# Optimization experiments

Hardware: AMD Instinct MI355X
Metric: run time of the kernel (lower is better)

## Reference

```python
import jax, jax.numpy as jnp
import numpy as np

WINDOW_SIZE = 11
SIGMA = 1.5
C1 = 0.01 ** 2
C2 = 0.03 ** 2


def _gaussian_window(size, sigma):
    coords = jnp.arange(size, dtype=jnp.float32) - (size - 1) / 2
    g = jnp.exp(-(coords ** 2) / (2 * sigma ** 2))
    g = g / g.sum()
    return g[:, None] * g[None, :]  # [size, size]


def _depthwise_conv(x, w2d):
    # x: [B, C, H, W]; w2d: [k, k] shared Gaussian window
    C = x.shape[1]
    k = w2d.shape[0]
    rhs = jnp.broadcast_to(w2d[None, None], (C, 1, k, k)).astype(x.dtype)
    pad = k // 2
    return jax.lax.conv_general_dilated(
        x, rhs,
        window_strides=(1, 1),
        padding=[(pad, pad), (pad, pad)],
        dimension_numbers=('NCHW', 'OIHW', 'NCHW'),
        feature_group_count=C,
    )


def setup_inputs() -> dict:
    key = jax.random.key(0)
    k1, k2 = jax.random.split(key)
    pred = jax.random.uniform(k1, (16, 3, 512, 512), dtype=jnp.float32)
    target = jax.random.uniform(k2, (16, 3, 512, 512), dtype=jnp.float32)
    return {"pred": pred, "target": target}


def reference(pred, target):
    w = _gaussian_window(WINDOW_SIZE, SIGMA)
    mu_x = _depthwise_conv(pred, w)
    mu_y = _depthwise_conv(target, w)
    s_x = _depthwise_conv(pred ** 2, w) - mu_x ** 2
    s_y = _depthwise_conv(target ** 2, w) - mu_y ** 2
    s_xy = _depthwise_conv(pred * target, w) - mu_x * mu_y
    ssim = ((2 * mu_x * mu_y + C1) * (2 * s_xy + C2)
            / ((mu_x ** 2 + mu_y ** 2 + C1) * (s_x + s_y + C2)))
    return 1.0 - ssim.mean()
```

## Files before the change

### kernel.cpp

```cpp
#include <hip/hip_runtime.h>
#include <math.h>

#define IMG_H 512
#define IMG_W 512
#define NPLANE 48
#define NXT 8
#define NSEG 8
#define NTASK (NPLANE*NXT*NSEG)
#define NPIX 12582912.0

__global__ void ssim_zero_kernel(double* acc) {
    if (threadIdx.x == 0) acc[0] = 0.0;
}

__global__ __launch_bounds__(256)
void ssim_main_kernel(const float* __restrict__ pred,
                      const float* __restrict__ targ,
                      double* __restrict__ acc,
                      float w0, float w1, float w2,
                      float w3, float w4, float w5) {
    const int wid  = (blockIdx.x << 2) + (threadIdx.x >> 6);
    const int lane = threadIdx.x & 63;
    const int xt   = wid & 7;
    const int yseg = (wid >> 3) & 7;
    const int pl   = wid >> 6;
    const int x    = (xt << 6) + lane;
    const int y0   = yseg << 6;

    const float* __restrict__ pb = pred + (size_t)pl * (IMG_H * IMG_W);
    const float* __restrict__ tb = targ + (size_t)pl * (IMG_H * IMG_W);

#define WSYM(M) ((M)==0||(M)==10 ? w0 : (M)==1||(M)==9 ? w1 :               \
                 (M)==2||(M)==8  ? w2 : (M)==3||(M)==7 ? w3 :               \
                 (M)==4||(M)==6  ? w4 : w5)

#define DECL_TAP(K)                                                          \
    const int   cq##K = x + (K) - 5;                                         \
    const int   cx##K = cq##K < 0 ? 0 : (cq##K > IMG_W - 1 ? IMG_W - 1 : cq##K); \
    const float wv##K = ((unsigned)cq##K < (unsigned)IMG_W) ? WSYM(K) : 0.f;
    DECL_TAP(0) DECL_TAP(1) DECL_TAP(2) DECL_TAP(3) DECL_TAP(4) DECL_TAP(5)
    DECL_TAP(6) DECL_TAP(7) DECL_TAP(8) DECL_TAP(9) DECL_TAP(10)
#undef DECL_TAP

#define DECL_RING(F) float F##0, F##1, F##2, F##3, F##4, F##5, F##6, F##7, F##8, F##9, F##10;
    DECL_RING(rmx) DECL_RING(rmy) DECL_RING(rxx) DECL_RING(ryy) DECL_RING(rxy)
#undef DECL_RING

#define HTAP(K) {                                                            \
    const float p  = pr[cx##K];                                              \
    const float t  = tr[cx##K];                                              \
    const float wp = wv##K * p;                                              \
    const float wt = wv##K * t;                                              \
    amx += wp; amy += wt;                                                    \
    axx = fmaf(wp, p, axx);                                                  \
    ayy = fmaf(wt, t, ayy);                                                  \
    axy = fmaf(wp, t, axy); }

#define HROW(YV, S) do {                                                     \
    const int y_ = (YV);                                                     \
    float amx = 0.f, amy = 0.f, axx = 0.f, ayy = 0.f, axy = 0.f;             \
    if ((unsigned)y_ < (unsigned)IMG_H) {           \
        const float* __restrict__ pr = pb + y_ * IMG_W;                      \
        const float* __restrict__ tr = tb + y_ * IMG_W;                      \
        HTAP(0) HTAP(1) HTAP(2) HTAP(3) HTAP(4) HTAP(5)                      \
        HTAP(6) HTAP(7) HTAP(8) HTAP(9) HTAP(10)                             \
    }                                                                        \
    rmx##S = amx; rmy##S = amy;                                              \
    rxx##S = axx; ryy##S = ayy; rxy##S = axy;                                \
} while (0)

    HROW(y0 - 5, 0); __builtin_amdgcn_sched_barrier(0);
    HROW(y0 - 4, 1); __builtin_amdgcn_sched_barrier(0);
    HROW(y0 - 3, 2); __builtin_amdgcn_sched_barrier(0);
    HROW(y0 - 2, 3); __builtin_amdgcn_sched_barrier(0);
    HROW(y0 - 1, 4); __builtin_amdgcn_sched_barrier(0);
    HROW(y0 + 0, 5); __builtin_amdgcn_sched_barrier(0);
    HROW(y0 + 1, 6); __builtin_amdgcn_sched_barrier(0);
    HROW(y0 + 2, 7); __builtin_amdgcn_sched_barrier(0);
    HROW(y0 + 3, 8); __builtin_amdgcn_sched_barrier(0);
    HROW(y0 + 4, 9); __builtin_amdgcn_sched_barrier(0);

    const float C1 = 0.0001f;
    const float C2 = 0.0009f;
    float sum = 0.f;

#define VTAP(JJ, S) {                                                        \
    const float wk = WSYM(((S) + 11 - (JJ)) % 11);                           \
    mx = fmaf(wk, rmx##S, mx);                                               \
    my = fmaf(wk, rmy##S, my);                                               \
    xx = fmaf(wk, rxx##S, xx);                                               \
    yy = fmaf(wk, ryy##S, yy);                                               \
    xy = fmaf(wk, rxy##S, xy); }

#define PHASE(JJ, SNEW) do {                                                 \
    const int j_ = c * 11 + (JJ);                                            \
    HROW(y0 + 5 + j_, SNEW);                                                 \
    float mx = 0.f, my = 0.f, xx = 0.f, yy = 0.f, xy = 0.f;                  \
    VTAP(JJ, 0) VTAP(JJ, 1) VTAP(JJ, 2) VTAP(JJ, 3) VTAP(JJ, 4) VTAP(JJ, 5)  \
    VTAP(JJ, 6) VTAP(JJ, 7) VTAP(JJ, 8) VTAP(JJ, 9) VTAP(JJ, 10)             \
    const float mx2  = mx * mx, my2 = my * my;                               \
    const float mxy2 = 2.f * (mx * my);                                      \
    const float sx   = xx - mx2, sy = yy - my2;                              \
    const float sxy2 = 2.f * xy - mxy2;                                      \
    const float num  = (mxy2 + C1) * (sxy2 + C2);                            \
    const float den  = (mx2 + my2 + C1) * (sx + sy + C2);                    \
    sum += (j_ < 64) ? __fdividef(num, den) : 0.f;                           \
    __builtin_amdgcn_sched_barrier(0);                                       \
} while (0)

#pragma unroll 1
    for (int c = 0; c < 6; ++c) {
        PHASE(0, 10); PHASE(1, 0); PHASE(2, 1); PHASE(3, 2); PHASE(4, 3);
        PHASE(5, 4);  PHASE(6, 5); PHASE(7, 6); PHASE(8, 7); PHASE(9, 8);
        PHASE(10, 9);
    }

#undef PHASE
#undef VTAP
#undef HROW
#undef HTAP
#undef WSYM

#pragma unroll
    for (int m = 32; m > 0; m >>= 1) sum += __shfl_xor(sum, m);
    if (lane == 0) atomicAdd(acc, (double)sum);
}

__global__ void ssim_fin_kernel(const double* __restrict__ acc, float* __restrict__ out) {
    out[0] = (float)(1.0 - acc[0] / NPIX);
}

extern "C" void kernel_launch(void* const* d_in, const int* in_sizes, int n_in,
                              void* d_out, int out_size, void* d_ws, size_t ws_size,
                              hipStream_t stream) {
    const float* pred = (const float*)d_in[0];
    const float* targ = (const float*)d_in[1];
    float* out  = (float*)d_out;
    double* acc = (double*)d_ws;

    double g[11], s = 0.0;
    for (int i = 0; i < 11; ++i) { double d = i - 5; g[i] = exp(-(d * d) / 4.5); s += g[i]; }
    float w[6];
    for (int i = 0; i < 6; ++i) w[i] = (float)(g[i] / s);

    ssim_zero_kernel<<<1, 64, 0, stream>>>(acc);
    ssim_main_kernel<<<NTASK / 4, 256, 0, stream>>>(pred, targ, acc,
                                                    w[0], w[1], w[2], w[3], w[4], w[5]);
    ssim_fin_kernel<<<1, 1, 0, stream>>>(acc, out);
}
```

Measured before the change: 262.1 us.

## Double-buffer row loads in registers and force uniform scalar base pointers

Result: faster. 255.5 us (-2.5%).

```diff
diff --git a/kernel.cpp b/kernel.cpp
--- a/kernel.cpp
+++ b/kernel.cpp
@@ -4,13 +4,18 @@
 #define IMG_H 512
 #define IMG_W 512
 #define NPLANE 48
-#define NXT 8
-#define NSEG 8
-#define NTASK (NPLANE*NXT*NSEG)
+#define NTASK (NPLANE*8*8)
 #define NPIX 12582912.0
 
 __global__ void ssim_zero_kernel(double* acc) {
     if (threadIdx.x == 0) acc[0] = 0.0;
+}
+
+__device__ __forceinline__ const float* uniform_ptr(const float* p) {
+    uint64_t u = (uint64_t)(uintptr_t)p;
+    uint32_t lo = __builtin_amdgcn_readfirstlane((uint32_t)u);
+    uint32_t hi = __builtin_amdgcn_readfirstlane((uint32_t)(u >> 32));
+    return (const float*)(uintptr_t)(((uint64_t)hi << 32) | (uint64_t)lo);
 }
 
 __global__ __launch_bounds__(256)
@@ -25,100 +30,115 @@
     const int yseg = (wid >> 3) & 7;
     const int pl   = wid >> 6;
     const int x    = (xt << 6) + lane;
-    const int y0   = yseg << 6;
+    const int y0u  = __builtin_amdgcn_readfirstlane(yseg << 6);
 
-    const float* __restrict__ pb = pred + (size_t)pl * (IMG_H * IMG_W);
-    const float* __restrict__ tb = targ + (size_t)pl * (IMG_H * IMG_W);
+    const float* pbu = uniform_ptr(pred + (size_t)pl * (IMG_H * IMG_W));
+    const float* tbu = uniform_ptr(targ + (size_t)pl * (IMG_H * IMG_W));
 
 #define WSYM(M) ((M)==0||(M)==10 ? w0 : (M)==1||(M)==9 ? w1 :               \
                  (M)==2||(M)==8  ? w2 : (M)==3||(M)==7 ? w3 :               \
                  (M)==4||(M)==6  ? w4 : w5)
 
 #define DECL_TAP(K)                                                          \
-    const int   cq##K = x + (K) - 5;                                         \
-    const int   cx##K = cq##K < 0 ? 0 : (cq##K > IMG_W - 1 ? IMG_W - 1 : cq##K); \
-    const float wv##K = ((unsigned)cq##K < (unsigned)IMG_W) ? WSYM(K) : 0.f;
+    const int      cq##K = x + (K) - 5;                                      \
+    const unsigned co##K = (unsigned)(cq##K < 0 ? 0 :                        \
+                           (cq##K > IMG_W - 1 ? IMG_W - 1 : cq##K));         \
+    const float    wv##K = ((unsigned)cq##K < (unsigned)IMG_W) ? WSYM(K) : 0.f;
     DECL_TAP(0) DECL_TAP(1) DECL_TAP(2) DECL_TAP(3) DECL_TAP(4) DECL_TAP(5)
     DECL_TAP(6) DECL_TAP(7) DECL_TAP(8) DECL_TAP(9) DECL_TAP(10)
 #undef DECL_TAP
 
-#define DECL_RING(F) float F##0, F##1, F##2, F##3, F##4, F##5, F##6, F##7, F##8, F##9, F##10;
+#define DECL_BUF(B) float B##p0,B##p1,B##p2,B##p3,B##p4,B##p5,B##p6,B##p7,  \
+                          B##p8,B##p9,B##p10,                               \
+                          B##t0,B##t1,B##t2,B##t3,B##t4,B##t5,B##t6,B##t7,  \
+                          B##t8,B##t9,B##t10;
+    DECL_BUF(A) DECL_BUF(B)
+#undef DECL_BUF
+
+#define DECL_RING(F) float F##0=0.f,F##1=0.f,F##2=0.f,F##3=0.f,F##4=0.f,     \
+                           F##5=0.f,F##6=0.f,F##7=0.f,F##8=0.f,F##9=0.f,F##10=0.f;
     DECL_RING(rmx) DECL_RING(rmy) DECL_RING(rxx) DECL_RING(ryy) DECL_RING(rxy)
 #undef DECL_RING
 
-#define HTAP(K) {                                                            \
-    const float p  = pr[cx##K];                                              \
-    const float t  = tr[cx##K];                                              \
-    const float wp = wv##K * p;                                              \
-    const float wt = wv##K * t;                                              \
-    amx += wp; amy += wt;                                                    \
-    axx = fmaf(wp, p, axx);                                                  \
-    ayy = fmaf(wt, t, ayy);                                                  \
-    axy = fmaf(wp, t, axy); }
-
-#define HROW(YV, S) do {                                                     \
-    const int y_ = (YV);                                                     \
-    float amx = 0.f, amy = 0.f, axx = 0.f, ayy = 0.f, axy = 0.f;             \
-    if ((unsigned)y_ < (unsigned)IMG_H) {           \
-        const float* __restrict__ pr = pb + y_ * IMG_W;                      \
-        const float* __restrict__ tr = tb + y_ * IMG_W;                      \
-        HTAP(0) HTAP(1) HTAP(2) HTAP(3) HTAP(4) HTAP(5)                      \
-        HTAP(6) HTAP(7) HTAP(8) HTAP(9) HTAP(10)                             \
-    }                                                                        \
-    rmx##S = amx; rmy##S = amy;                                              \
-    rxx##S = axx; ryy##S = ayy; rxy##S = axy;                                \
+#define LR1(BUF, K) BUF##p##K = rp_[co##K]; BUF##t##K = rt_[co##K];
+#define LOADROW(BUF, IDX) do {                                               \
+    const int yq_ = y0u - 5 + (IDX);                                         \
+    const int yc_ = yq_ < 0 ? 0 : (yq_ > IMG_H - 1 ? IMG_H - 1 : yq_);       \
+    const float* rp_ = pbu + yc_ * IMG_W;                                    \
+    const float* rt_ = tbu + yc_ * IMG_W;                                    \
+    LR1(BUF,0) LR1(BUF,1) LR1(BUF,2) LR1(BUF,3) LR1(BUF,4) LR1(BUF,5)        \
+    LR1(BUF,6) LR1(BUF,7) LR1(BUF,8) LR1(BUF,9) LR1(BUF,10)                  \
 } while (0)
 
-    HROW(y0 - 5, 0); __builtin_amdgcn_sched_barrier(0);
-    HROW(y0 - 4, 1); __builtin_amdgcn_sched_barrier(0);
-    HROW(y0 - 3, 2); __builtin_amdgcn_sched_barrier(0);
-    HROW(y0 - 2, 3); __builtin_amdgcn_sched_barrier(0);
-    HROW(y0 - 1, 4); __builtin_amdgcn_sched_barrier(0);
-    HROW(y0 + 0, 5); __builtin_amdgcn_sched_barrier(0);
-    HROW(y0 + 1, 6); __builtin_amdgcn_sched_barrier(0);
-    HROW(y0 + 2, 7); __builtin_amdgcn_sched_barrier(0);
-    HROW(y0 + 3, 8); __builtin_amdgcn_sched_barrier(0);
-    HROW(y0 + 4, 9); __builtin_amdgcn_sched_barrier(0);
+#define HT(BUF, K) {                                                         \
+    const float p_ = BUF##p##K, t_ = BUF##t##K;                              \
+    const float wp_ = wv##K * p_, wt_ = wv##K * t_;                          \
+    amx += wp_; amy += wt_;                                                  \
+    axx = fmaf(wp_, p_, axx);                                                \
+    ayy = fmaf(wt_, t_, ayy);                                                \
+    axy = fmaf(wp_, t_, axy); }
+
+#define VT(Q11, S) {                                                         \
+    const float wk_ = WSYM(((S) + 10 - (Q11)) % 11);                         \
+    mx = fmaf(wk_, rmx##S, mx);                                              \
+    my = fmaf(wk_, rmy##S, my);                                              \
+    xx = fmaf(wk_, rxx##S, xx);                                              \
+    yy = fmaf(wk_, ryy##S, yy);                                              \
+    xy = fmaf(wk_, rxy##S, xy); }
 
     const float C1 = 0.0001f;
     const float C2 = 0.0009f;
     float sum = 0.f;
 
-#define VTAP(JJ, S) {                                                        \
-    const float wk = WSYM(((S) + 11 - (JJ)) % 11);                           \
-    mx = fmaf(wk, rmx##S, mx);                                               \
-    my = fmaf(wk, rmy##S, my);                                               \
-    xx = fmaf(wk, rxx##S, xx);                                               \
-    yy = fmaf(wk, ryy##S, yy);                                               \
-    xy = fmaf(wk, rxy##S, xy); }
-
-#define PHASE(JJ, SNEW) do {                                                 \
-    const int j_ = c * 11 + (JJ);                                            \
-    HROW(y0 + 5 + j_, SNEW);                                                 \
-    float mx = 0.f, my = 0.f, xx = 0.f, yy = 0.f, xy = 0.f;                  \
-    VTAP(JJ, 0) VTAP(JJ, 1) VTAP(JJ, 2) VTAP(JJ, 3) VTAP(JJ, 4) VTAP(JJ, 5)  \
-    VTAP(JJ, 6) VTAP(JJ, 7) VTAP(JJ, 8) VTAP(JJ, 9) VTAP(JJ, 10)             \
-    const float mx2  = mx * mx, my2 = my * my;                               \
-    const float mxy2 = 2.f * (mx * my);                                      \
-    const float sx   = xx - mx2, sy = yy - my2;                              \
-    const float sxy2 = 2.f * xy - mxy2;                                      \
-    const float num  = (mxy2 + C1) * (sxy2 + C2);                            \
-    const float den  = (mx2 + my2 + C1) * (sx + sy + C2);                    \
-    sum += (j_ < 64) ? __fdividef(num, den) : 0.f;                           \
-    __builtin_amdgcn_sched_barrier(0);                                       \
+#define PHASE(IDXE, Q11, BC, BN) do {                                        \
+    LOADROW(BN, (IDXE) + 1);                                                 \
+    {                                                                        \
+        float amx=0.f, amy=0.f, axx=0.f, ayy=0.f, axy=0.f;                   \
+        HT(BC,0) HT(BC,1) HT(BC,2) HT(BC,3) HT(BC,4) HT(BC,5)                \
+        HT(BC,6) HT(BC,7) HT(BC,8) HT(BC,9) HT(BC,10)                        \
+        const bool vld_ = (unsigned)(y0u - 5 + (IDXE)) < (unsigned)IMG_H;    \
+        rmx##Q11 = vld_ ? amx : 0.f;  rmy##Q11 = vld_ ? amy : 0.f;           \
+        rxx##Q11 = vld_ ? axx : 0.f;  ryy##Q11 = vld_ ? ayy : 0.f;           \
+        rxy##Q11 = vld_ ? axy : 0.f;                                         \
+    }                                                                        \
+    {                                                                        \
+        float mx=0.f, my=0.f, xx=0.f, yy=0.f, xy=0.f;                        \
+        VT(Q11,0) VT(Q11,1) VT(Q11,2) VT(Q11,3) VT(Q11,4) VT(Q11,5)          \
+        VT(Q11,6) VT(Q11,7) VT(Q11,8) VT(Q11,9) VT(Q11,10)                   \
+        const float mx2  = mx * mx, my2 = my * my;                           \
+        const float mxy2 = 2.f * (mx * my);                                  \
+        const float sx   = xx - mx2, sy = yy - my2;                          \
+        const float sxy2 = 2.f * xy - mxy2;                                  \
+        const float num  = (mxy2 + C1) * (sxy2 + C2);                        \
+        const float den  = (mx2 + my2 + C1) * (sx + sy + C2);                \
+        const int   j_   = (IDXE) - 10;                                      \
+        sum += (j_ >= 0) ? __fdividef(num, den) : 0.f;                       \
+    }                                                                        \
+    __builtin_amdgcn_sched_barrier(0x7);     \
 } while (0)
 
+    LOADROW(A, 0);
+
 #pragma unroll 1
-    for (int c = 0; c < 6; ++c) {
-        PHASE(0, 10); PHASE(1, 0); PHASE(2, 1); PHASE(3, 2); PHASE(4, 3);
-        PHASE(5, 4);  PHASE(6, 5); PHASE(7, 6); PHASE(8, 7); PHASE(9, 8);
-        PHASE(10, 9);
+    for (int cc = 0; cc < 3; ++cc) {
+        const int ib = cc * 22;
+        PHASE(ib+0 ,0 ,A,B); PHASE(ib+1 ,1 ,B,A); PHASE(ib+2 ,2 ,A,B);
+        PHASE(ib+3 ,3 ,B,A); PHASE(ib+4 ,4 ,A,B); PHASE(ib+5 ,5 ,B,A);
+        PHASE(ib+6 ,6 ,A,B); PHASE(ib+7 ,7 ,B,A); PHASE(ib+8 ,8 ,A,B);
+        PHASE(ib+9 ,9 ,B,A); PHASE(ib+10,10,A,B); PHASE(ib+11,0 ,B,A);
+        PHASE(ib+12,1 ,A,B); PHASE(ib+13,2 ,B,A); PHASE(ib+14,3 ,A,B);
+        PHASE(ib+15,4 ,B,A); PHASE(ib+16,5 ,A,B); PHASE(ib+17,6 ,B,A);
+        PHASE(ib+18,7 ,A,B); PHASE(ib+19,8 ,B,A); PHASE(ib+20,9 ,A,B);
+        PHASE(ib+21,10,B,A);
     }
+    PHASE(66,0,A,B); PHASE(67,1,B,A); PHASE(68,2,A,B); PHASE(69,3,B,A);
+    PHASE(70,4,A,B); PHASE(71,5,B,A); PHASE(72,6,A,B); PHASE(73,7,B,A);
 
 #undef PHASE
-#undef VTAP
-#undef HROW
-#undef HTAP
+#undef VT
+#undef HT
+#undef LOADROW
+#undef LR1
 #undef WSYM
 
 #pragma unroll
```
